# Kernel tuning notes

Hardware: AMD Instinct MI355X
Metric: run time of the kernel (lower is better)

Reference implementation:

```python
import jax, jax.numpy as jnp
import numpy as np
import math

B, S, D, NS, K, V = 4, 1024, 256, 64, 16, 32000
NEG = -10000.0


def l2n(x, axis=-1):
    # F.normalize with eps=1e-12
    return x / jnp.maximum(jnp.linalg.norm(x, axis=axis, keepdims=True), 1e-12)


def sparsemax(z, axis=-1):
    # sort descending, find support size k_z, threshold tau
    z_sorted = -jnp.sort(-z, axis=axis)
    cumsum = jnp.cumsum(z_sorted, axis=axis)
    n = z.shape[axis]
    k = jnp.arange(1, n + 1, dtype=z.dtype).reshape((1,) * (z.ndim - 1) + (n,))
    check = (1.0 + k * z_sorted > cumsum).astype(z.dtype)
    k_z = jnp.sum(check, axis=axis, keepdims=True)
    tau = (jnp.take_along_axis(cumsum, (k_z - 1).astype(jnp.int32), axis=axis) - 1.0) / k_z
    return jnp.maximum(z - tau, 0.0)


def router_forward(messages, hidden, x_ids, scn, mask, static_nb, geo_velocity,
                   ctx_conf, current_entropy, vel_proj_w, edge_w1, edge_b1,
                   edge_w2, edge_b2, probe_w, geo_gate_w, geo_gate_b):
    S_ = messages.shape[1]
    dg = jnp.eye(S_, dtype=bool)
    mfull = mask[None] | dg[None]  # masked_fill(mask) + diagonal fill combined

    # --- geodesic-endpoint routed attention ---
    endpoint = l2n(scn + 0.4 * geo_velocity)                      # [B,S,NS]
    endpoint_sim = jnp.einsum('bsn,btn->bst', endpoint, scn)      # [B,S,S]
    endpoint_sim = jnp.where(mfull, NEG, endpoint_sim)
    H_norm = jax.lax.stop_gradient(current_entropy)[..., None] / (math.log(V) + 1e-8)
    vel_h = geo_velocity @ vel_proj_w.T                           # [B,S,D]
    h_aimed = l2n(hidden + 0.3 * vel_h)
    h_msg_sim = jnp.einsum('bsd,btd->bst', h_aimed, messages)
    combined_geo = (endpoint_sim * H_norm + 0.5 * h_msg_sim) * 5.0
    combined_geo = jnp.where(mfull, NEG, combined_geo)
    ew_geo = sparsemax(combined_geo, axis=-1)
    geo_agg = jnp.einsum('bst,btd->bsd', ew_geo, messages)

    # --- vocab-neighbor match / aggregate ---
    nb_vocab = static_nb[x_ids]                                   # [B,S,K]
    match = (x_ids[:, None, None, :] == nb_vocab[..., None]).astype(messages.dtype)  # [B,S,K,S]
    causal = jnp.tril(jnp.ones((S_, S_), messages.dtype))
    match = match * causal[None, :, None, :]
    coverage = jnp.mean(jnp.minimum(jnp.sum(match, -1), 1.0), axis=-1, keepdims=True)  # [B,S,1]
    nb_msgs_s = jnp.einsum('bskp,bpd->bskd', match, messages)
    nb_scn_s = jnp.einsum('bskp,bpn->bskn', match, scn)
    sim_s = jnp.sum(nb_scn_s * scn[:, :, None, :], -1)            # [B,S,K]
    e = jax.nn.gelu(sim_s[..., None] @ edge_w1.T + edge_b1, approximate=False)
    e = (e @ edge_w2.T + edge_b2)[..., 0]
    ew_s = jax.nn.softmax(e, axis=-1)
    static_agg = jnp.sum(nb_msgs_s * ew_s[..., None], axis=2)     # [B,S,D]

    # --- local same-mode routing with sparsemax ---
    my_mode = jnp.argmax(scn, -1)
    same_mode = (my_mode[:, :, None] == my_mode[:, None, :]).astype(messages.dtype)
    same_mode = jnp.where(mfull, 0.0, same_mode)
    scn_sim = jnp.einsum('bsn,btn->bst', scn, scn) * same_mode
    has_nb = jnp.sum(same_mode, -1, keepdims=True) > 0
    pos = jnp.arange(S_, dtype=messages.dtype)
    pos_sim = -jnp.abs(pos[:, None] - pos[None, :])[None]
    pos_sim = jnp.where(mfull, NEG, pos_sim)
    routing_sim = jnp.where(has_nb, scn_sim, pos_sim * 0.01)
    routing_sim = jnp.where(mfull, NEG, routing_sim)
    ew_l = sparsemax(routing_sim * 5.0, axis=-1)
    local_agg = jnp.einsum('bst,btd->bsd', ew_l, messages)

    static_final = coverage * static_agg + (1.0 - coverage) * local_agg
    raw_gate = jax.nn.sigmoid(hidden @ geo_gate_w.T + geo_gate_b)
    geo_weight = raw_gate * ctx_conf
    agg = geo_weight * geo_agg + (1.0 - geo_weight) * static_final
    probe = l2n(hidden @ probe_w.T)
    agg_n = l2n(agg)
    rel = jax.nn.sigmoid(jnp.sum(agg_n * probe, -1, keepdims=True))
    return agg * rel


def setup_inputs() -> dict:
    key = jax.random.key(0)
    ks = jax.random.split(key, 14)
    messages = jax.random.normal(ks[0], (B, S, D), jnp.float32)
    hidden = jax.random.normal(ks[1], (B, S, D), jnp.float32)
    x_ids = jax.random.randint(ks[2], (B, S), 0, V)
    scn = jax.random.normal(ks[3], (B, S, NS), jnp.float32)
    mask = ~jnp.tril(jnp.ones((S, S), bool))  # True above diagonal (disallowed)
    static_nb = jax.random.randint(ks[4], (V, K), 0, V)
    geo_velocity = jax.random.normal(ks[5], (B, S, NS), jnp.float32) * 0.5
    ctx_conf = jax.random.uniform(ks[6], (B, S, 1), jnp.float32)
    current_entropy = jax.random.uniform(ks[7], (B, S), jnp.float32) * math.log(V)
    vel_proj_w = jax.random.normal(ks[8], (D, NS), jnp.float32) / np.sqrt(NS).astype(np.float32)
    edge_w1 = jax.random.normal(ks[9], (8, 1), jnp.float32)
    edge_b1 = jnp.zeros((8,), jnp.float32)
    edge_w2 = jax.random.normal(ks[10], (1, 8), jnp.float32) * 0.3
    edge_b2 = jnp.zeros((1,), jnp.float32)
    probe_w = jax.random.normal(ks[11], (D, D), jnp.float32) / np.sqrt(D).astype(np.float32)
    geo_gate_w = jax.random.normal(ks[12], (1, D), jnp.float32) * 0.02
    geo_gate_b = jnp.full((1,), -4.0, jnp.float32)
    return dict(messages=messages, hidden=hidden, x_ids=x_ids, scn=scn, mask=mask,
                static_nb=static_nb, geo_velocity=geo_velocity, ctx_conf=ctx_conf,
                current_entropy=current_entropy, vel_proj_w=vel_proj_w,
                edge_w1=edge_w1, edge_b1=edge_b1, edge_w2=edge_w2, edge_b2=edge_b2,
                probe_w=probe_w, geo_gate_w=geo_gate_w, geo_gate_b=geo_gate_b)


def reference(messages, hidden, x_ids, scn, mask, static_nb, geo_velocity, ctx_conf,
              current_entropy, vel_proj_w, edge_w1, edge_b1, edge_w2, edge_b2,
              probe_w, geo_gate_w, geo_gate_b):
    return router_forward(messages, hidden, x_ids, scn, mask, static_nb, geo_velocity,
                          ctx_conf, current_entropy, vel_proj_w, edge_w1, edge_b1,
                          edge_w2, edge_b2, probe_w, geo_gate_w, geo_gate_b)
```

## Files before the change

kernel.cpp:

```cpp
#include <hip/hip_runtime.h>
#include <math.h>

#define B_ 4
#define S_ 1024
#define D_ 256
#define NS_ 64
#define KNB 16
#define KPACK 320
#define NEG_ (-10000.0f)
#define LOGV_INV (1.0f/(10.373491181781864f + 1e-8f))
#define MCAP 64
#define NCHUNK 16
#define SUPCAP 1024

typedef __attribute__((ext_vector_type(8))) short short8;
typedef __attribute__((ext_vector_type(8))) unsigned short ushort8v;
typedef __attribute__((ext_vector_type(4))) float f32x4;


__device__ __forceinline__ void blockReduceSum4(float4& v, float* red) {
  #pragma unroll
  for (int off = 32; off > 0; off >>= 1) {
    v.x += __shfl_down(v.x, off, 64);
    v.y += __shfl_down(v.y, off, 64);
    v.z += __shfl_down(v.z, off, 64);
    v.w += __shfl_down(v.w, off, 64);
  }
  int lane = threadIdx.x & 63;
  int w = threadIdx.x >> 6;
  __syncthreads();
  if (lane == 0) {
    red[w] = v.x; red[4 + w] = v.y; red[8 + w] = v.z; red[12 + w] = v.w;
  }
  __syncthreads();
  v.x = red[0] + red[1] + red[2] + red[3];
  v.y = red[4] + red[5] + red[6] + red[7];
  v.z = red[8] + red[9] + red[10] + red[11];
  v.w = red[12] + red[13] + red[14] + red[15];
}

__device__ __forceinline__ void waveAllSum2(float& a, float& b) {
  #pragma unroll
  for (int off = 1; off < 64; off <<= 1) {
    a += __shfl_xor(a, off, 64);
    b += __shfl_xor(b, off, 64);
  }
}

__device__ __forceinline__ float michelot_tau16(const float* z) {
  float m = z[0];
  #pragma unroll
  for (int k = 1; k < 16; k++) m = fmaxf(m, z[k]);
  #pragma unroll
  for (int off = 1; off < 64; off <<= 1) m = fmaxf(m, __shfl_xor(m, off, 64));
  float thr = m - 1.0f;
  float s = 0.f, c = 0.f;
  #pragma unroll
  for (int k = 0; k < 16; k++) { float zk = z[k]; if (zk > thr) { s += zk; c += 1.f; } }
  waveAllSum2(s, c);
  int cnt = (int)c;
  float tau = (s - 1.0f) / c;
  for (int it = 0; it < 32; ++it) {
    float s2 = 0.f, c2 = 0.f;
    #pragma unroll
    for (int k = 0; k < 16; k++) { float zk = z[k]; if (zk > tau) { s2 += zk; c2 += 1.f; } }
    waveAllSum2(s2, c2);
    int ci = (int)c2;
    if (ci == cnt || ci == 0) break;
    cnt = ci;
    tau = (s2 - 1.0f) / c2;
  }
  return tau;
}

__device__ __forceinline__ unsigned short f2bf_rne(float f) {
  union { float f; unsigned u; } v; v.f = f;
  unsigned r = v.u + 0x7FFFu + ((v.u >> 16) & 1u);
  return (unsigned short)(r >> 16);
}
__device__ __forceinline__ float bf2f(unsigned short h) {
  union { unsigned u; float f; } v; v.u = ((unsigned)h) << 16;
  return v.f;
}
__device__ __forceinline__ void cvt_store4(unsigned short* hi, unsigned short* lo, float4 v) {
  unsigned short h0 = f2bf_rne(v.x), h1 = f2bf_rne(v.y), h2 = f2bf_rne(v.z), h3 = f2bf_rne(v.w);
  *(ushort4*)hi = make_ushort4(h0, h1, h2, h3);
  *(ushort4*)lo = make_ushort4(f2bf_rne(v.x - bf2f(h0)), f2bf_rne(v.y - bf2f(h1)),
                               f2bf_rne(v.z - bf2f(h2)), f2bf_rne(v.w - bf2f(h3)));
}
#define MFMA16(a,b,c) __builtin_amdgcn_mfma_f32_16x16x32_bf16((a),(b),(c),0,0,0)


__global__ __launch_bounds__(256) void bf16_split_kernel(
    const float* __restrict__ messages, const float* __restrict__ hidden,
    const float* __restrict__ scn, const float* __restrict__ gv,
    const float* __restrict__ probe_w, const float* __restrict__ vel_w,
    unsigned short* __restrict__ msg_hi, unsigned short* __restrict__ msg_lo,
    unsigned short* __restrict__ hid_hi, unsigned short* __restrict__ hid_lo,
    unsigned short* __restrict__ scn_hi, unsigned short* __restrict__ scn_lo,
    unsigned short* __restrict__ gv_hi,  unsigned short* __restrict__ gv_lo,
    unsigned short* __restrict__ pw_hi,  unsigned short* __restrict__ pw_lo,
    unsigned short* __restrict__ vw_hi,  unsigned short* __restrict__ vw_lo)
{
  const float* src; unsigned short *hi, *lo; int n;
  switch (blockIdx.y) {
    case 0: src = messages; hi = msg_hi; lo = msg_lo; n = B_*S_*D_;  break;
    case 1: src = hidden;   hi = hid_hi; lo = hid_lo; n = B_*S_*D_;  break;
    case 2: src = scn;      hi = scn_hi; lo = scn_lo; n = B_*S_*NS_; break;
    case 3: src = gv;       hi = gv_hi;  lo = gv_lo;  n = B_*S_*NS_; break;
    case 4: src = probe_w;  hi = pw_hi;  lo = pw_lo;  n = D_*D_;     break;
    default: src = vel_w;   hi = vw_hi;  lo = vw_lo;  n = D_*NS_;    break;
  }
  int idx = (blockIdx.x * 256 + threadIdx.x) * 4;
  if (idx >= n) return;
  float4 v = *(const float4*)(src + idx);
  cvt_store4(hi + idx, lo + idx, v);
}


__global__ __launch_bounds__(256) void msum_partial_kernel(
    const float* __restrict__ messages, float* __restrict__ part)
{
  int blk = blockIdx.x;
  int b = blk >> 4, c = blk & 15;
  int d = threadIdx.x;
  const float* src = messages + ((size_t)b * S_ + c * 64) * D_ + d;
  float acc = 0.f;
  #pragma unroll 8
  for (int t = 0; t < 64; t++) acc += src[t * D_];
  part[((size_t)b * NCHUNK + c) * D_ + d] = acc;
}

#define LDB 40


__global__ __launch_bounds__(256) void dual_gemm_mfma_kernel(
    const unsigned short* __restrict__ hid_hi, const unsigned short* __restrict__ hid_lo,
    const unsigned short* __restrict__ gv_hi,  const unsigned short* __restrict__ gv_lo,
    const unsigned short* __restrict__ pw_hi,  const unsigned short* __restrict__ pw_lo,
    const unsigned short* __restrict__ vw_hi,  const unsigned short* __restrict__ vw_lo,
    float* __restrict__ probe_raw, float* __restrict__ vel_h)
{
  __shared__ unsigned short Ahi[64][LDB], Alo[64][LDB];
  __shared__ unsigned short Bhi[64][LDB], Blo[64][LDB];
  int which = blockIdx.y;
  const unsigned short* Ah = which ? gv_hi : hid_hi;
  const unsigned short* Al = which ? gv_lo : hid_lo;
  const unsigned short* Wh = which ? vw_hi : pw_hi;
  const unsigned short* Wl = which ? vw_lo : pw_lo;
  float* C = which ? vel_h : probe_raw;
  int K = which ? NS_ : D_;

  int mt = blockIdx.x >> 2, nt4 = blockIdx.x & 3;
  int s0 = mt * 64, t0 = nt4 * 64;
  int tid = threadIdx.x, lane = tid & 63, w = tid >> 6;
  int fm = lane & 15, fq = lane >> 4;
  int si = tid >> 2, sc = tid & 3;

  f32x4 acc[4];
  #pragma unroll
  for (int i = 0; i < 4; i++) acc[i] = (f32x4){0.f, 0.f, 0.f, 0.f};

  for (int k0 = 0; k0 < K; k0 += 32) {
    *(ushort8v*)&Ahi[si][sc*8] = *(const ushort8v*)(Ah + (size_t)(s0 + si) * K + k0 + sc*8);
    *(ushort8v*)&Alo[si][sc*8] = *(const ushort8v*)(Al + (size_t)(s0 + si) * K + k0 + sc*8);
    *(ushort8v*)&Bhi[si][sc*8] = *(const ushort8v*)(Wh + (size_t)(t0 + si) * K + k0 + sc*8);
    *(ushort8v*)&Blo[si][sc*8] = *(const ushort8v*)(Wl + (size_t)(t0 + si) * K + k0 + sc*8);
    __syncthreads();
    short8 ah = *(const short8*)&Ahi[w*16 + fm][fq*8];
    short8 al = *(const short8*)&Alo[w*16 + fm][fq*8];
    #pragma unroll
    for (int nt = 0; nt < 4; nt++) {
      short8 bh = *(const short8*)&Bhi[nt*16 + fm][fq*8];
      short8 bl = *(const short8*)&Blo[nt*16 + fm][fq*8];
      acc[nt] = MFMA16(ah, bh, acc[nt]);
      acc[nt] = MFMA16(ah, bl, acc[nt]);
      acc[nt] = MFMA16(al, bh, acc[nt]);
    }
    __syncthreads();
  }

  #pragma unroll
  for (int nt = 0; nt < 4; nt++)
    #pragma unroll
    for (int rg = 0; rg < 4; rg++)
      C[(size_t)(s0 + w*16 + fq*4 + rg) * D_ + t0 + nt*16 + fm] = acc[nt][rg];
}


__global__ __launch_bounds__(256) void prep3_kernel(
    const float* __restrict__ hidden,
    const float* __restrict__ scn, const float* __restrict__ gv,
    const float* __restrict__ ctx_conf, const float* __restrict__ entropy,
    const float* __restrict__ probe_raw, const float* __restrict__ vel_h,
    const float* __restrict__ gate_w, const float* __restrict__ gate_b,
    unsigned short* __restrict__ arow_hi, unsigned short* __restrict__ arow_lo,
    float* __restrict__ probe, float* __restrict__ gw_out,
    int* __restrict__ mode_out)
{
  int r = blockIdx.x;
  int tid = threadIdx.x;
  __shared__ float sh_scn[NS_];
  __shared__ float red[16];

  float sv = 0.f, gvv = 0.f;
  if (tid < NS_) {
    sv  = scn[(size_t)r*NS_ + tid];
    gvv = gv[(size_t)r*NS_ + tid];
    sh_scn[tid] = sv;
  }
  float hid = hidden[(size_t)r*D_ + tid];
  float vh  = vel_h[(size_t)r*D_ + tid];
  float pr  = probe_raw[(size_t)r*D_ + tid];
  float gwt = gate_w[tid];

  float ep = (tid < NS_) ? (sv + 0.4f*gvv) : 0.f;
  float ha = hid + 0.3f*vh;

  float4 v = make_float4(ep*ep, ha*ha, pr*pr, hid*gwt);
  blockReduceSum4(v, red);

  float Hn = entropy[r] * LOGV_INV;
  float epn = fmaxf(sqrtf(v.x), 1e-12f);
  float han = fmaxf(sqrtf(v.y), 1e-12f);
  float prn = fmaxf(sqrtf(v.z), 1e-12f);

  if (tid < NS_) {
    float v0 = (5.0f*Hn) * (ep / epn);
    unsigned short h = f2bf_rne(v0);
    arow_hi[(size_t)r*KPACK + tid] = h;
    arow_lo[(size_t)r*KPACK + tid] = f2bf_rne(v0 - bf2f(h));
  }
  {
    float v1 = 2.5f * (ha / han);
    unsigned short h = f2bf_rne(v1);
    arow_hi[(size_t)r*KPACK + NS_ + tid] = h;
    arow_lo[(size_t)r*KPACK + NS_ + tid] = f2bf_rne(v1 - bf2f(h));
  }
  probe[(size_t)r*D_ + tid] = pr / prn;

  if (tid == 0) {
    float rg = 1.f/(1.f + expf(-(v.w + gate_b[0])));
    gw_out[r] = rg * ctx_conf[r];
    float m = sh_scn[0]; int mi = 0;
    for (int n = 1; n < NS_; n++) { if (sh_scn[n] > m) { m = sh_scn[n]; mi = n; } }
    mode_out[r] = mi;
  }
}


#define GBT 64
#define GBK 32
#define NTRI 136

__global__ __launch_bounds__(256) void geo_gemm_mfma2_kernel(
    const unsigned short* __restrict__ arow_hi, const unsigned short* __restrict__ arow_lo,
    const unsigned short* __restrict__ scn_hi,  const unsigned short* __restrict__ scn_lo,
    const unsigned short* __restrict__ msg_hi,  const unsigned short* __restrict__ msg_lo,
    float* __restrict__ z, float* __restrict__ sim)
{
  __shared__ unsigned short Ahi[GBT][LDB], Alo[GBT][LDB];
  __shared__ unsigned short Bhi[GBT][LDB], Blo[GBT][LDB];
  __shared__ unsigned short A2hi[GBT][LDB], A2lo[GBT][LDB];

  int blk = blockIdx.x;
  int b = blk / NTRI;
  int tri = blk % NTRI;
  int ts = 0;
  while ((ts + 1) * (ts + 2) / 2 <= tri) ts++;
  int tt = tri - ts * (ts + 1) / 2;
  int s0 = ts * GBT, t0 = tt * GBT;

  const unsigned short* Ah = arow_hi + (size_t)b * S_ * KPACK;
  const unsigned short* Al = arow_lo + (size_t)b * S_ * KPACK;
  const unsigned short* Sh = scn_hi + (size_t)b * S_ * NS_;
  const unsigned short* Sl = scn_lo + (size_t)b * S_ * NS_;
  const unsigned short* Mh = msg_hi + (size_t)b * S_ * D_;
  const unsigned short* Ml = msg_lo + (size_t)b * S_ * D_;

  int tid = threadIdx.x, lane = tid & 63, w = tid >> 6;
  int fm = lane & 15, fq = lane >> 4;
  int si = tid >> 2, sc = tid & 3;

  f32x4 accz[4], accs[4];
  #pragma unroll
  for (int i = 0; i < 4; i++) {
    accz[i] = (f32x4){0.f, 0.f, 0.f, 0.f};
    accs[i] = (f32x4){0.f, 0.f, 0.f, 0.f};
  }

  for (int k0 = 0; k0 < KPACK; k0 += GBK) {
    bool scn_slab = (k0 < NS_);
    *(ushort8v*)&Ahi[si][sc*8] = *(const ushort8v*)(Ah + (size_t)(s0 + si) * KPACK + k0 + sc*8);
    *(ushort8v*)&Alo[si][sc*8] = *(const ushort8v*)(Al + (size_t)(s0 + si) * KPACK + k0 + sc*8);
    if (scn_slab) {
      *(ushort8v*)&Bhi[si][sc*8]  = *(const ushort8v*)(Sh + (size_t)(t0 + si) * NS_ + k0 + sc*8);
      *(ushort8v*)&Blo[si][sc*8]  = *(const ushort8v*)(Sl + (size_t)(t0 + si) * NS_ + k0 + sc*8);
      *(ushort8v*)&A2hi[si][sc*8] = *(const ushort8v*)(Sh + (size_t)(s0 + si) * NS_ + k0 + sc*8);
      *(ushort8v*)&A2lo[si][sc*8] = *(const ushort8v*)(Sl + (size_t)(s0 + si) * NS_ + k0 + sc*8);
    } else {
      *(ushort8v*)&Bhi[si][sc*8] = *(const ushort8v*)(Mh + (size_t)(t0 + si) * D_ + (k0 - NS_) + sc*8);
      *(ushort8v*)&Blo[si][sc*8] = *(const ushort8v*)(Ml + (size_t)(t0 + si) * D_ + (k0 - NS_) + sc*8);
    }
    __syncthreads();

    short8 ah = *(const short8*)&Ahi[w*16 + fm][fq*8];
    short8 al = *(const short8*)&Alo[w*16 + fm][fq*8];
    short8 a2h, a2l;
    if (scn_slab) {
      a2h = *(const short8*)&A2hi[w*16 + fm][fq*8];
      a2l = *(const short8*)&A2lo[w*16 + fm][fq*8];
    }
    #pragma unroll
    for (int nt = 0; nt < 4; nt++) {
      short8 bh = *(const short8*)&Bhi[nt*16 + fm][fq*8];
      short8 bl = *(const short8*)&Blo[nt*16 + fm][fq*8];
      accz[nt] = MFMA16(ah, bh, accz[nt]);
      accz[nt] = MFMA16(ah, bl, accz[nt]);
      accz[nt] = MFMA16(al, bh, accz[nt]);
      if (scn_slab) {
        accs[nt] = MFMA16(a2h, bh, accs[nt]);
        accs[nt] = MFMA16(a2h, bl, accs[nt]);
        accs[nt] = MFMA16(a2l, bh, accs[nt]);
      }
    }
    __syncthreads();
  }

  float* zb = z + (size_t)b * S_ * S_;
  float* sb = sim + (size_t)b * S_ * S_;
  #pragma unroll
  for (int nt = 0; nt < 4; nt++) {
    #pragma unroll
    for (int rg = 0; rg < 4; rg++) {
      int row = s0 + w*16 + fq*4 + rg;
      int col = t0 + nt*16 + fm;
      zb[(size_t)row * S_ + col] = accz[nt][rg];
      sb[(size_t)row * S_ + col] = accs[nt][rg];
    }
  }
}


__global__ __launch_bounds__(256) void rows_fused8_kernel(
    const float* __restrict__ zbuf, const float* __restrict__ simbuf,
    const float* __restrict__ messages, const int* __restrict__ mode,
    const int* __restrict__ x_ids, const int* __restrict__ static_nb,
    const float* __restrict__ ew1, const float* __restrict__ eb1,
    const float* __restrict__ ew2, const float* __restrict__ eb2,
    const float* __restrict__ gw, const float* __restrict__ probe,
    const float* __restrict__ part, float* __restrict__ out)
{
  __shared__ int xb_l[S_];
  __shared__ int mode_l[S_];
  __shared__ unsigned short gt_l[2][SUPCAP];
  __shared__ float gw_l[2][SUPCAP];
  __shared__ unsigned short lt_l[2][SUPCAP];
  __shared__ float lw_l[2][SUPCAP];
  __shared__ int gcnt_s[2], lcnt_s[2];
  __shared__ unsigned short mk_s[2][MCAP];
  __shared__ unsigned short mp_s[2][MCAP];
  __shared__ float ews[2][KNB];
  __shared__ float cov_s[2];
  __shared__ int M_s[2];
  __shared__ float red2[2][2][2];

  const int tid = threadIdx.x;
  const int lane = tid & 63;
  const int wv = tid >> 6;
  const int rw = wv >> 1;
  const int half = wv & 1;
  const int r = blockIdx.x * 2 + rw;
  const int b = r >> 10, s = r & 1023;
  const unsigned long long lmask_lt = (1ull << lane) - 1ull;

  const float2* msg2 = (const float2*)(messages + (size_t)b * S_ * D_);
  const int dbase = half * 64 + lane;

  ((int4*)xb_l)[tid]   = ((const int4*)(x_ids + (size_t)b * S_))[tid];
  ((int4*)mode_l)[tid] = ((const int4*)(mode + (size_t)b * S_))[tid];
  __syncthreads();

  if (half == 0) {
    if (s != 0) {
      const float4* zrow4 = (const float4*)(zbuf + (size_t)r * S_);
      float zg[16];
      #pragma unroll
      for (int j = 0; j < 4; j++) {
        int t0 = j*256 + lane*4;
        if (j*256 < s) {
          float4 v = zrow4[j*64 + lane];
          zg[j*4+0] = (t0+0 < s) ? v.x : NEG_;
          zg[j*4+1] = (t0+1 < s) ? v.y : NEG_;
          zg[j*4+2] = (t0+2 < s) ? v.z : NEG_;
          zg[j*4+3] = (t0+3 < s) ? v.w : NEG_;
        } else {
          zg[j*4+0] = NEG_; zg[j*4+1] = NEG_; zg[j*4+2] = NEG_; zg[j*4+3] = NEG_;
        }
      }
      float tau = michelot_tau16(zg);
      int base = 0;
      #pragma unroll
      for (int k = 0; k < 16; k++) {
        float w = zg[k] - tau;
        bool p = w > 0.f;
        unsigned long long m = __ballot(p);
        if (p) {
          int idx = base + __popcll(m & lmask_lt);
          gt_l[rw][idx] = (unsigned short)((k >> 2)*256 + lane*4 + (k & 3));
          gw_l[rw][idx] = w;
        }
        base += __popcll(m);
      }
      if (lane == 0) gcnt_s[rw] = base;
    } else if (lane == 0) gcnt_s[rw] = 0;

    int xid = xb_l[s];
    int nb[KNB];
    #pragma unroll
    for (int k = 0; k < KNB; k++) nb[k] = static_nb[(size_t)xid * KNB + k];
    float simk[KNB];
    #pragma unroll
    for (int k = 0; k < KNB; k++) simk[k] = 0.f;
    unsigned int kmask = 0;
    int M = 0;
    for (int j = 0; j < 16; j++) {
      int p = j*64 + lane;
      int xp = xb_l[p];
      bool anym = false;
      #pragma unroll
      for (int k = 0; k < KNB; k++) anym |= (nb[k] == xp);
      anym = anym && (p <= s);
      float d_self = 0.f;
      if (anym) d_self = simbuf[(size_t)r * S_ + p];
      unsigned long long m = __ballot(anym);
      while (m) {
        int ln = __ffsll((unsigned long long)m) - 1; m &= m - 1;
        int pp = j*64 + ln;
        int xpp = xb_l[pp];
        float d = __shfl(d_self, ln, 64);
        #pragma unroll
        for (int k = 0; k < KNB; k++) {
          if (nb[k] == xpp) {
            if (M < MCAP && lane == 0) { mk_s[rw][M] = (unsigned short)k; mp_s[rw][M] = (unsigned short)pp; }
            M++;
            simk[k] += d;
            kmask |= (1u << k);
          }
        }
      }
    }
    if (M > MCAP) M = MCAP;
    if (lane == 0) { M_s[rw] = M; cov_s[rw] = (float)__popc(kmask) * (1.0f/(float)KNB); }
    if (M > 0) {
      if (lane == 0) {
        #pragma unroll
        for (int k = 0; k < KNB; k++) ews[rw][k] = simk[k];
      }
      float sim = (lane < KNB) ? ews[rw][lane] : 0.f;
      float e = eb2[0];
      #pragma unroll
      for (int j = 0; j < 8; j++) {
        float x = sim * ew1[j] + eb1[j];
        float gx = 0.5f * x * (1.0f + erff(x * 0.70710678118654752f));
        e += gx * ew2[j];
      }
      float mx = e;
      #pragma unroll
      for (int off = 1; off < 16; off <<= 1) mx = fmaxf(mx, __shfl_xor(mx, off, 64));
      float ex = expf(e - mx);
      float ssum = ex;
      #pragma unroll
      for (int off = 1; off < 16; off <<= 1) ssum += __shfl_xor(ssum, off, 64);
      if (lane < KNB) ews[rw][lane] = ex / ssum;
    }
  } else {
    if (s != 0) {
      int mode_s = mode_l[s];
      int cnt = 0;
      unsigned int pmask = 0;
      #pragma unroll
      for (int j = 0; j < 16; j++) {
        int t = j*64 + lane;
        bool p = (t < s) && (mode_l[t] == mode_s);
        if (p) pmask |= (1u << j);
        cnt += __popcll(__ballot(p));
      }
      bool has_nb = cnt > 0;
      float zl[16];
      #pragma unroll
      for (int j = 0; j < 16; j++) {
        int t = j*64 + lane;
        float zv;
        if (t >= s) zv = NEG_ * 5.0f;
        else if (pmask & (1u << j)) zv = simbuf[(size_t)r * S_ + t] * 5.0f;
        else if (has_nb) zv = 0.f;
        else zv = (0.01f * (-(float)(s - t))) * 5.0f;
        zl[j] = zv;
      }
      float tau = michelot_tau16(zl);
      int base = 0;
      #pragma unroll
      for (int j = 0; j < 16; j++) {
        float w = zl[j] - tau;
        bool p = w > 0.f;
        unsigned long long m = __ballot(p);
        if (p) {
          int idx = base + __popcll(m & lmask_lt);
          lt_l[rw][idx] = (unsigned short)(j*64 + lane);
          lw_l[rw][idx] = w;
        }
        base += __popcll(m);
      }
      if (lane == 0) lcnt_s[rw] = base;
    } else if (lane == 0) lcnt_s[rw] = 0;
  }
  __syncthreads();

  float2 accg = {0.f, 0.f}, accl = {0.f, 0.f}, accs = {0.f, 0.f};
  if (s == 0) {
    const float2* part2 = (const float2*)(part + (size_t)b * NCHUNK * D_);
    float2 msum = {0.f, 0.f};
    #pragma unroll
    for (int c = 0; c < NCHUNK; c++) {
      float2 pm = part2[c * 128 + dbase];
      msum.x += pm.x; msum.y += pm.y;
    }
    accg.x = 0.0009765625f * msum.x; accg.y = 0.0009765625f * msum.y;
    accl.x = 0.00390625f * msum.x;   accl.y = 0.00390625f * msum.y;
  } else {
    int gc = gcnt_s[rw];
    for (int i = 0; i < gc; i++) {
      float w = gw_l[rw][i];
      float2 mm = msg2[(size_t)gt_l[rw][i] * 128 + dbase];
      accg.x += w*mm.x; accg.y += w*mm.y;
    }
    int lc = lcnt_s[rw];
    for (int i = 0; i < lc; i++) {
      float w = lw_l[rw][i];
      float2 mm = msg2[(size_t)lt_l[rw][i] * 128 + dbase];
      accl.x += w*mm.x; accl.y += w*mm.y;
    }
  }
  {
    int M = M_s[rw];
    for (int i = 0; i < M; i++) {
      int k = mk_s[rw][i], p = mp_s[rw][i];
      float w = ews[rw][k];
      float2 mm = msg2[(size_t)p * 128 + dbase];
      accs.x += w*mm.x; accs.y += w*mm.y;
    }
  }

  float g = gw[r];
  float cov = cov_s[rw];
  float2 agg;
  agg.x = g*accg.x + (1.f-g)*(cov*accs.x + (1.f-cov)*accl.x);
  agg.y = g*accg.y + (1.f-g)*(cov*accs.y + (1.f-cov)*accl.y);

  float2 pv = ((const float2*)probe)[(size_t)r * 128 + dbase];
  float n2 = agg.x*agg.x + agg.y*agg.y;
  float ap = agg.x*pv.x + agg.y*pv.y;
  waveAllSum2(n2, ap);
  if (lane == 0) { red2[rw][half][0] = n2; red2[rw][half][1] = ap; }
  __syncthreads();
  n2 = red2[rw][0][0] + red2[rw][1][0];
  ap = red2[rw][0][1] + red2[rw][1][1];
  float nrm = fmaxf(sqrtf(n2), 1e-12f);
  float rel = 1.f / (1.f + expf(-(ap / nrm)));
  float2 o;
  o.x = agg.x * rel; o.y = agg.y * rel;
  ((float2*)out)[(size_t)r * 128 + dbase] = o;
}


extern "C" void kernel_launch(void* const* d_in, const int* in_sizes, int n_in,
                              void* d_out, int out_size, void* d_ws, size_t ws_size,
                              hipStream_t stream)
{
  const float* messages  = (const float*)d_in[0];
  const float* hidden    = (const float*)d_in[1];
  const int*   x_ids     = (const int*)d_in[2];
  const float* scn       = (const float*)d_in[3];
  const int*   static_nb = (const int*)d_in[5];
  const float* gv        = (const float*)d_in[6];
  const float* ctx_conf  = (const float*)d_in[7];
  const float* entropy   = (const float*)d_in[8];
  const float* vel_w     = (const float*)d_in[9];
  const float* ew1       = (const float*)d_in[10];
  const float* eb1       = (const float*)d_in[11];
  const float* ew2       = (const float*)d_in[12];
  const float* eb2       = (const float*)d_in[13];
  const float* probe_w   = (const float*)d_in[14];
  const float* gate_w    = (const float*)d_in[15];
  const float* gate_b    = (const float*)d_in[16];
  float* out = (float*)d_out;

  float* ws = (float*)d_ws;
  float* probe   = ws;
  float* gwbuf   = probe + (size_t)B_*S_*D_;
  int*   mode    = (int*)(gwbuf + (size_t)B_*S_);
  float* zbuf    = (float*)(mode + (size_t)B_*S_);
  float* simbuf  = zbuf + (size_t)B_*S_*S_;
  float* vel_h   = simbuf + (size_t)B_*S_*S_;
  float* part    = vel_h + (size_t)B_*S_*D_;
  unsigned short* msg_hi  = (unsigned short*)(part + (size_t)B_*NCHUNK*D_);
  unsigned short* msg_lo  = msg_hi  + (size_t)B_*S_*D_;
  unsigned short* scn_hi  = msg_lo  + (size_t)B_*S_*D_;
  unsigned short* scn_lo  = scn_hi  + (size_t)B_*S_*NS_;
  unsigned short* arow_hi = scn_lo  + (size_t)B_*S_*NS_;
  unsigned short* arow_lo = arow_hi + (size_t)B_*S_*KPACK;
  unsigned short* hid_hi = (unsigned short*)zbuf;
  unsigned short* hid_lo = hid_hi + (size_t)B_*S_*D_;
  unsigned short* gv_hi  = hid_lo + (size_t)B_*S_*D_;
  unsigned short* gv_lo  = gv_hi  + (size_t)B_*S_*NS_;
  unsigned short* pw_hi  = gv_lo  + (size_t)B_*S_*NS_;
  unsigned short* pw_lo  = pw_hi  + (size_t)D_*D_;
  unsigned short* vw_hi  = pw_lo  + (size_t)D_*D_;
  unsigned short* vw_lo  = vw_hi  + (size_t)D_*NS_;

  bf16_split_kernel<<<dim3(1024, 6), dim3(256), 0, stream>>>(
      messages, hidden, scn, gv, probe_w, vel_w,
      msg_hi, msg_lo, hid_hi, hid_lo, scn_hi, scn_lo,
      gv_hi, gv_lo, pw_hi, pw_lo, vw_hi, vw_lo);

  msum_partial_kernel<<<dim3(B_*NCHUNK), dim3(256), 0, stream>>>(messages, part);

  dual_gemm_mfma_kernel<<<dim3(256, 2), dim3(256), 0, stream>>>(
      hid_hi, hid_lo, gv_hi, gv_lo, pw_hi, pw_lo, vw_hi, vw_lo,
      probe, vel_h);

  prep3_kernel<<<dim3(B_*S_), dim3(256), 0, stream>>>(
      hidden, scn, gv, ctx_conf, entropy, probe, vel_h,
      gate_w, gate_b, arow_hi, arow_lo, probe, gwbuf, mode);

  geo_gemm_mfma2_kernel<<<dim3(B_*NTRI), dim3(256), 0, stream>>>(
      arow_hi, arow_lo, scn_hi, scn_lo, msg_hi, msg_lo, zbuf, simbuf);

  rows_fused8_kernel<<<dim3(B_*S_/2), dim3(256), 0, stream>>>(
      zbuf, simbuf, messages, mode, x_ids, static_nb,
      ew1, eb1, ew2, eb2, gwbuf, probe, part, out);
}
```

Before: 180.2 us.

## Use prefix-sum partials for dense local sparsemax aggregation instead of per-support gather

When the local sparsemax support is large (most preceding tokens have zero logit with a small set of same-mode neighbours), the weighted aggregation is rewritten as -tau times the prefix sum of messages, computed from per-64-row chunk partials plus a tail, plus a correction over the few same-mode positions. This replaces hundreds of per-row message gathers with up to 16 partial reads, a short tail loop and a small correction loop. It assumes every non-neighbour logit equals zero and sits inside the support. It adds a shared-memory list of same-mode indices and falls back to the original loop when the conditions fail.

New measurement: 170.0 us. 5.7% less time.

```diff
diff --git a/kernel.cpp b/kernel.cpp
--- a/kernel.cpp
+++ b/kernel.cpp
@@ -12,6 +12,7 @@
 #define MCAP 64
 #define NCHUNK 16
 #define SUPCAP 1024
+#define SMC 128
 
 typedef __attribute__((ext_vector_type(8))) short short8;
 typedef __attribute__((ext_vector_type(8))) unsigned short ushort8v;
@@ -342,7 +343,7 @@
 }
 
 
-__global__ __launch_bounds__(256) void rows_fused8_kernel(
+__global__ __launch_bounds__(256) void rows_fused10_kernel(
     const float* __restrict__ zbuf, const float* __restrict__ simbuf,
     const float* __restrict__ messages, const int* __restrict__ mode,
     const int* __restrict__ x_ids, const int* __restrict__ static_nb,
@@ -357,7 +358,9 @@
   __shared__ float gw_l[2][SUPCAP];
   __shared__ unsigned short lt_l[2][SUPCAP];
   __shared__ float lw_l[2][SUPCAP];
-  __shared__ int gcnt_s[2], lcnt_s[2];
+  __shared__ unsigned short sm_l[2][SMC];
+  __shared__ int gcnt_s[2], lcnt_s[2], smcnt_s[2];
+  __shared__ float taul_s[2];
   __shared__ unsigned short mk_s[2][MCAP];
   __shared__ unsigned short mp_s[2][MCAP];
   __shared__ float ews[2][KNB];
@@ -477,16 +480,22 @@
   } else {
     if (s != 0) {
       int mode_s = mode_l[s];
-      int cnt = 0;
+      int smcnt = 0;
       unsigned int pmask = 0;
       #pragma unroll
       for (int j = 0; j < 16; j++) {
         int t = j*64 + lane;
         bool p = (t < s) && (mode_l[t] == mode_s);
-        if (p) pmask |= (1u << j);
-        cnt += __popcll(__ballot(p));
-      }
-      bool has_nb = cnt > 0;
+        unsigned long long m = __ballot(p);
+        if (p) {
+          pmask |= (1u << j);
+          int idx = smcnt + __popcll(m & lmask_lt);
+          if (idx < SMC) sm_l[rw][idx] = (unsigned short)t;
+        }
+        smcnt += __popcll(m);
+      }
+      bool has_nb = smcnt > 0;
+      if (lane == 0) smcnt_s[rw] = smcnt;
       float zl[16];
       #pragma unroll
       for (int j = 0; j < 16; j++) {
@@ -499,6 +508,7 @@
         zl[j] = zv;
       }
       float tau = michelot_tau16(zl);
+      if (lane == 0) taul_s[rw] = tau;
       int base = 0;
       #pragma unroll
       for (int j = 0; j < 16; j++) {
@@ -513,13 +523,13 @@
         base += __popcll(m);
       }
       if (lane == 0) lcnt_s[rw] = base;
-    } else if (lane == 0) lcnt_s[rw] = 0;
+    } else if (lane == 0) { lcnt_s[rw] = 0; smcnt_s[rw] = 0; }
   }
   __syncthreads();
 
   float2 accg = {0.f, 0.f}, accl = {0.f, 0.f}, accs = {0.f, 0.f};
+  const float2* part2 = (const float2*)(part + (size_t)b * NCHUNK * D_);
   if (s == 0) {
-    const float2* part2 = (const float2*)(part + (size_t)b * NCHUNK * D_);
     float2 msum = {0.f, 0.f};
     #pragma unroll
     for (int c = 0; c < NCHUNK; c++) {
@@ -536,10 +546,35 @@
       accg.x += w*mm.x; accg.y += w*mm.y;
     }
     int lc = lcnt_s[rw];
-    for (int i = 0; i < lc; i++) {
-      float w = lw_l[rw][i];
-      float2 mm = msg2[(size_t)lt_l[rw][i] * 128 + dbase];
-      accl.x += w*mm.x; accl.y += w*mm.y;
+    int smc = smcnt_s[rw];
+    if (lc >= 256 && smc >= 1 && smc <= SMC) {
+      float taul = taul_s[rw];
+      float w0 = -taul;
+      float2 psum = {0.f, 0.f};
+      int nc = s >> 6;
+      for (int c = 0; c < nc; c++) {
+        float2 pm = part2[c * 128 + dbase];
+        psum.x += pm.x; psum.y += pm.y;
+      }
+      for (int t = nc * 64; t < s; t++) {
+        float2 mm = msg2[(size_t)t * 128 + dbase];
+        psum.x += mm.x; psum.y += mm.y;
+      }
+      accl.x = w0 * psum.x; accl.y = w0 * psum.y;
+      const float* simrow = simbuf + (size_t)r * S_;
+      for (int i = 0; i < smc; i++) {
+        int t = sm_l[rw][i];
+        float sv5 = simrow[t] * 5.0f;
+        float corr = (sv5 - taul > 0.f) ? sv5 : taul;
+        float2 mm = msg2[(size_t)t * 128 + dbase];
+        accl.x += corr * mm.x; accl.y += corr * mm.y;
+      }
+    } else {
+      for (int i = 0; i < lc; i++) {
+        float w = lw_l[rw][i];
+        float2 mm = msg2[(size_t)lt_l[rw][i] * 128 + dbase];
+        accl.x += w*mm.x; accl.y += w*mm.y;
+      }
     }
   }
   {
@@ -637,7 +672,7 @@
   geo_gemm_mfma2_kernel<<<dim3(B_*NTRI), dim3(256), 0, stream>>>(
       arow_hi, arow_lo, scn_hi, scn_lo, msg_hi, msg_lo, zbuf, simbuf);
 
-  rows_fused8_kernel<<<dim3(B_*S_/2), dim3(256), 0, stream>>>(
+  rows_fused10_kernel<<<dim3(B_*S_/2), dim3(256), 0, stream>>>(
       zbuf, simbuf, messages, mode, x_ids, static_nb,
       ew1, eb1, ew2, eb2, gwbuf, probe, part, out);
 }
```
